# Performance work log

Measured on AMD Instinct MI355X. Metric: run time of the kernel, lower is better.

## Reference

```python
import jax, jax.numpy as jnp
import numpy as np

U_FEAT = 100000  # user feature vocab
I_FEAT = 100000  # item feature vocab
D = 64           # embedding dim
N_USERS = 4096   # batch of users
N_ITEMS = 16384  # all items
L_U = 50         # nonzero features per user
L_I = 20         # nonzero features per item


def setup_inputs() -> dict:
    key = jax.random.key(0)
    ks = jax.random.split(key, 9)
    return {
        "user_features_embeddings": jax.random.normal(ks[0], (U_FEAT, D), jnp.float32),
        "item_features_embeddings": jax.random.normal(ks[1], (I_FEAT, D), jnp.float32),
        "user_w": jax.random.normal(ks[2], (U_FEAT,), jnp.float32),
        "item_w": jax.random.normal(ks[3], (I_FEAT,), jnp.float32),
        "global_bias": jax.random.normal(ks[4], (1,), jnp.float32),
        "h1": jax.random.normal(ks[5], (D,), jnp.float32),
        "h2": jax.random.normal(ks[6], (D,), jnp.float32),
        "user_idx": jax.random.randint(ks[7], (N_USERS, L_U), 0, U_FEAT),
        "item_idx": jax.random.randint(ks[8], (N_ITEMS, L_I), 0, I_FEAT),
    }


def _pooled(emb, idx, w, h1):
    # emb: [V, D], idx: [N, L], w: [V]
    g = emb[idx]                                   # [N, L, D] gather
    s = g.sum(axis=1)                              # [N, D] feature-embedding sum
    # FM bi-interaction: 0.5 * (sum^2 - sum of squares)
    bi = 0.5 * (jnp.square(s) - jnp.square(g).sum(axis=1))  # [N, D]
    scalar = bi @ h1 + w[idx].sum(axis=1)          # [N]
    return s, scalar


def reference(user_features_embeddings, item_features_embeddings, user_w, item_w,
              global_bias, h1, h2, user_idx, item_idx):
    su, sc_u = _pooled(user_features_embeddings, user_idx, user_w, h1)
    si, sc_i = _pooled(item_features_embeddings, item_idx, item_w, h1)
    ones_u = jnp.ones((su.shape[0], 1), su.dtype)
    ones_i = jnp.ones((si.shape[0], 1), si.dtype)
    # p_u = [sum_emb, h1.bi + sum(w) + bias, 1]; q_v = [sum_emb, 1, h1.bi + sum(w)]
    P = jnp.concatenate([su, (sc_u + global_bias[0])[:, None], ones_u], axis=1)  # [N_USERS, D+2]
    Q = jnp.concatenate([si, ones_i, sc_i[:, None]], axis=1)                     # [N_ITEMS, D+2]
    return P, Q, h2
```

## Files before the change

kernel.cpp:

```cpp
#include <hip/hip_runtime.h>

#define EMB_D 64
#define NU 4096
#define NI 16384
#define LDOUT (EMB_D + 2)

__device__ __forceinline__ float4 ld4(const float* p) {
  return *reinterpret_cast<const float4*>(p);
}

template<int L>
__device__ __forceinline__ void fm_row(const float* __restrict__ emb,
                                       const float* __restrict__ w,
                                       const int* __restrict__ idx, int row,
                                       const float* __restrict__ h1,
                                       float bias, float* __restrict__ out,
                                       int scalar_col, int one_col, int lane) {
  const int* ridx = idx + (size_t)row * L;
  const int g = lane >> 4;
  const int sub = lane & 15;

  int myidx = (lane < L) ? ridx[lane] : 0;

  const char* base = (const char*)emb;

  float4 s  = make_float4(0.f, 0.f, 0.f, 0.f);
  float4 sq = make_float4(0.f, 0.f, 0.f, 0.f);

  constexpr int LM = L & ~3;
#pragma unroll
  for (int l = 0; l < LM; l += 4) {
    int id = __shfl(myidx, l + g, 64);
    unsigned boff = ((unsigned)id << 8) | (unsigned)(sub << 4);
    float4 e = ld4((const float*)(base + boff));
    s.x += e.x; s.y += e.y; s.z += e.z; s.w += e.w;
    sq.x += e.x * e.x; sq.y += e.y * e.y; sq.z += e.z * e.z; sq.w += e.w * e.w;
  }
  if constexpr (LM != L) {
    constexpr int TAIL = L - LM;
    int srcl = LM + (g < TAIL ? g : 0);
    int id = __shfl(myidx, srcl, 64);
    if (g < TAIL) {
      unsigned boff = ((unsigned)id << 8) | (unsigned)(sub << 4);
      float4 e = ld4((const float*)(base + boff));
      s.x += e.x; s.y += e.y; s.z += e.z; s.w += e.w;
      sq.x += e.x * e.x; sq.y += e.y * e.y; sq.z += e.z * e.z; sq.w += e.w * e.w;
    }
  }

#pragma unroll
  for (int off = 16; off <= 32; off <<= 1) {
    s.x += __shfl_xor(s.x, off, 64);  s.y += __shfl_xor(s.y, off, 64);
    s.z += __shfl_xor(s.z, off, 64);  s.w += __shfl_xor(s.w, off, 64);
  }

  float4 h = ld4(h1 + sub * 4);
  float part = -0.5f * (sq.x * h.x + sq.y * h.y + sq.z * h.z + sq.w * h.w);
  if (g == 0)
    part += 0.5f * (s.x * s.x * h.x + s.y * s.y * h.y +
                    s.z * s.z * h.z + s.w * s.w * h.w);
  if (lane < L) part += w[myidx];

#pragma unroll
  for (int off = 32; off >= 1; off >>= 1) part += __shfl_down(part, off, 64);

  float* orow = out + (size_t)row * LDOUT;
  if (g == 0) {
    *reinterpret_cast<float2*>(orow + sub * 4)     = make_float2(s.x, s.y);
    *reinterpret_cast<float2*>(orow + sub * 4 + 2) = make_float2(s.z, s.w);
  }
  if (lane == 0) {
    orow[scalar_col] = part + bias;
    orow[one_col]    = 1.0f;
  }
}

__global__ __launch_bounds__(256) void fm_fused(
    const float* __restrict__ uemb, const float* __restrict__ iemb,
    const float* __restrict__ uw, const float* __restrict__ iw,
    const float* __restrict__ gb, const float* __restrict__ h1,
    const float* __restrict__ h2, const int* __restrict__ uidx,
    const int* __restrict__ iidx, float* __restrict__ out) {
  int wid  = blockIdx.x * 4 + (threadIdx.x >> 6);
  int lane = threadIdx.x & 63;

  float* P  = out;
  float* Q  = P + (size_t)NU * LDOUT;
  float* H2 = Q + (size_t)NI * LDOUT;

  if (wid < NU) {
    fm_row<50>(uemb, uw, uidx, wid, h1, gb[0], P, 64, 65, lane);
  } else if (wid < NU + NI) {
    fm_row<20>(iemb, iw, iidx, wid - NU, h1, 0.f, Q, 65, 64, lane);
  } else if (wid == NU + NI) {
    H2[lane] = h2[lane];
  }
}

extern "C" void kernel_launch(void* const* d_in, const int* in_sizes, int n_in,
                              void* d_out, int out_size, void* d_ws, size_t ws_size,
                              hipStream_t stream) {
  const float* uemb = (const float*)d_in[0];
  const float* iemb = (const float*)d_in[1];
  const float* uw   = (const float*)d_in[2];
  const float* iw   = (const float*)d_in[3];
  const float* gb   = (const float*)d_in[4];
  const float* h1   = (const float*)d_in[5];
  const float* h2   = (const float*)d_in[6];
  const int*   uidx = (const int*)d_in[7];
  const int*   iidx = (const int*)d_in[8];

  int nwaves = NU + NI + 1;
  int nblocks = (nwaves + 3) / 4;

  fm_fused<<<dim3(nblocks), dim3(256), 0, stream>>>(
      uemb, iemb, uw, iw, gb, h1, h2, uidx, iidx, (float*)d_out);
}
```

Measured before the change: 25.58 us.

## Process two item rows per wavefront to fill all lanes

Item rows have only 20 features, so one wavefront per row left many lanes idle and issued 5 iterations with 4 groups. The change packs two item rows per 64-lane wavefront, each half handling 10 iterations of 2 gathers, which halves the number of item wavefronts. This raises lane utilization and cuts per-wave overhead (index loads, reductions), but lengthens each wave's dependent load chain.

```diff
diff --git a/kernel.cpp b/kernel.cpp
--- a/kernel.cpp
+++ b/kernel.cpp
@@ -9,19 +9,18 @@
   return *reinterpret_cast<const float4*>(p);
 }
 
-template<int L>
-__device__ __forceinline__ void fm_row(const float* __restrict__ emb,
-                                       const float* __restrict__ w,
-                                       const int* __restrict__ idx, int row,
-                                       const float* __restrict__ h1,
-                                       float bias, float* __restrict__ out,
-                                       int scalar_col, int one_col, int lane) {
+__device__ __forceinline__ void fm_user_row(const float* __restrict__ emb,
+                                            const float* __restrict__ w,
+                                            const int* __restrict__ idx, int row,
+                                            const float* __restrict__ h1,
+                                            float bias, float* __restrict__ out,
+                                            int lane) {
+  constexpr int L = 50;
   const int* ridx = idx + (size_t)row * L;
   const int g = lane >> 4;
   const int sub = lane & 15;
 
   int myidx = (lane < L) ? ridx[lane] : 0;
-
   const char* base = (const char*)emb;
 
   float4 s  = make_float4(0.f, 0.f, 0.f, 0.f);
@@ -36,7 +35,7 @@
     s.x += e.x; s.y += e.y; s.z += e.z; s.w += e.w;
     sq.x += e.x * e.x; sq.y += e.y * e.y; sq.z += e.z * e.z; sq.w += e.w * e.w;
   }
-  if constexpr (LM != L) {
+  {
     constexpr int TAIL = L - LM;
     int srcl = LM + (g < TAIL ? g : 0);
     int id = __shfl(myidx, srcl, 64);
@@ -70,8 +69,60 @@
     *reinterpret_cast<float2*>(orow + sub * 4 + 2) = make_float2(s.z, s.w);
   }
   if (lane == 0) {
-    orow[scalar_col] = part + bias;
-    orow[one_col]    = 1.0f;
+    orow[64] = part + bias;
+    orow[65] = 1.0f;
+  }
+}
+
+__device__ __forceinline__ void fm_item_pair(const float* __restrict__ emb,
+                                             const float* __restrict__ w,
+                                             const int* __restrict__ idx, int pair,
+                                             const float* __restrict__ h1,
+                                             float* __restrict__ out, int lane) {
+  constexpr int L = 20;
+  const int r  = lane >> 5;
+  const int lr = lane & 31;
+  const int g2 = lr >> 4;
+  const int sub = lane & 15;
+  const int row = pair * 2 + r;
+
+  int myidx = (lr < L) ? idx[(size_t)row * L + lr] : 0;
+  const char* base = (const char*)emb;
+
+  float4 s  = make_float4(0.f, 0.f, 0.f, 0.f);
+  float4 sq = make_float4(0.f, 0.f, 0.f, 0.f);
+
+#pragma unroll
+  for (int k = 0; k < L / 2; ++k) {
+    int src = (r << 5) + 2 * k + g2;
+    int id = __shfl(myidx, src, 64);
+    unsigned boff = ((unsigned)id << 8) | (unsigned)(sub << 4);
+    float4 e = ld4((const float*)(base + boff));
+    s.x += e.x; s.y += e.y; s.z += e.z; s.w += e.w;
+    sq.x += e.x * e.x; sq.y += e.y * e.y; sq.z += e.z * e.z; sq.w += e.w * e.w;
+  }
+
+  s.x += __shfl_xor(s.x, 16, 64);  s.y += __shfl_xor(s.y, 16, 64);
+  s.z += __shfl_xor(s.z, 16, 64);  s.w += __shfl_xor(s.w, 16, 64);
+
+  float4 h = ld4(h1 + sub * 4);
+  float part = -0.5f * (sq.x * h.x + sq.y * h.y + sq.z * h.z + sq.w * h.w);
+  if (g2 == 0)
+    part += 0.5f * (s.x * s.x * h.x + s.y * s.y * h.y +
+                    s.z * s.z * h.z + s.w * s.w * h.w);
+  if (lr < L) part += w[myidx];
+
+#pragma unroll
+  for (int off = 16; off >= 1; off >>= 1) part += __shfl_xor(part, off, 64);
+
+  float* orow = out + (size_t)row * LDOUT;
+  if (g2 == 0) {
+    *reinterpret_cast<float2*>(orow + sub * 4)     = make_float2(s.x, s.y);
+    *reinterpret_cast<float2*>(orow + sub * 4 + 2) = make_float2(s.z, s.w);
+  }
+  if (lr == 0) {
+    orow[64] = 1.0f;
+    orow[65] = part;
   }
 }
 
@@ -89,10 +140,10 @@
   float* H2 = Q + (size_t)NI * LDOUT;
 
   if (wid < NU) {
-    fm_row<50>(uemb, uw, uidx, wid, h1, gb[0], P, 64, 65, lane);
-  } else if (wid < NU + NI) {
-    fm_row<20>(iemb, iw, iidx, wid - NU, h1, 0.f, Q, 65, 64, lane);
-  } else if (wid == NU + NI) {
+    fm_user_row(uemb, uw, uidx, wid, h1, gb[0], P, lane);
+  } else if (wid < NU + NI / 2) {
+    fm_item_pair(iemb, iw, iidx, wid - NU, h1, Q, lane);
+  } else if (wid == NU + NI / 2) {
     H2[lane] = h2[lane];
   }
 }
@@ -110,7 +161,7 @@
   const int*   uidx = (const int*)d_in[7];
   const int*   iidx = (const int*)d_in[8];
 
-  int nwaves = NU + NI + 1;
+  int nwaves = NU + NI / 2 + 1;
   int nblocks = (nwaves + 3) / 4;
 
   fm_fused<<<dim3(nblocks), dim3(256), 0, stream>>>(
```

After: 25.46 us. No clear change (-0.4%).
